# Optimization experiments

Measured on AMD Instinct MI355X. Metric: run time of the kernel, lower is better.

Reference implementation:

```python
import jax, jax.numpy as jnp
import numpy as np

EMBED = 1024
HEADS = 16
HEAD_DIM = EMBED // HEADS


def setup_inputs() -> dict:
    key = jax.random.key(0)
    ks = jax.random.split(key, 9)
    B, S = 1, 4096
    scale = 1.0 / np.sqrt(EMBED)
    x = jax.random.normal(ks[0], (B, S, EMBED), dtype=jnp.float32)
    # nn.Linear weights stored as [out, in]; we store transposed [in, out] for x @ W
    Wq = jax.random.uniform(ks[1], (EMBED, EMBED), jnp.float32, -scale, scale)
    bq = jax.random.uniform(ks[2], (EMBED,), jnp.float32, -scale, scale)
    Wk = jax.random.uniform(ks[3], (EMBED, EMBED), jnp.float32, -scale, scale)
    bk = jax.random.uniform(ks[4], (EMBED,), jnp.float32, -scale, scale)
    Wv = jax.random.uniform(ks[5], (EMBED, EMBED), jnp.float32, -scale, scale)
    bv = jax.random.uniform(ks[6], (EMBED,), jnp.float32, -scale, scale)
    Wo = jax.random.uniform(ks[7], (EMBED, EMBED), jnp.float32, -scale, scale)
    bo = jax.random.uniform(ks[8], (EMBED,), jnp.float32, -scale, scale)
    return {"x": x, "Wq": Wq, "bq": bq, "Wk": Wk, "bk": bk,
            "Wv": Wv, "bv": bv, "Wo": Wo, "bo": bo}


def reference(x, Wq, bq, Wk, bk, Wv, bv, Wo, bo):
    B, S, E = x.shape
    H, D = HEADS, HEAD_DIM
    # projections
    Q = (x @ Wq + bq).reshape(B, S, H, D).transpose(0, 2, 1, 3)  # [B,H,S,D]
    K = (x @ Wk + bk).reshape(B, S, H, D).transpose(0, 2, 1, 3)
    V = (x @ Wv + bv).reshape(B, S, H, D).transpose(0, 2, 1, 3)
    # unfused attention: full [B,H,S,S] score matrix, matching the torch module
    scores = jnp.einsum('bhqd,bhkd->bhqk', Q, K) / jnp.sqrt(jnp.float32(D)).astype(x.dtype)
    probs = jax.nn.softmax(scores, axis=-1)
    out = jnp.einsum('bhqk,bhkd->bhqd', probs, V)  # [B,H,S,D]
    out = out.transpose(0, 2, 1, 3).reshape(B, S, E)
    return out @ Wo + bo
```

## Files before the change

kernel.cpp:

```cpp
#include <hip/hip_runtime.h>


constexpr int Sq = 4096;
constexpr int Ee = 1024;
constexpr int Hh = 16;
constexpr int Dh = 64;

typedef _Float16 half8 __attribute__((ext_vector_type(8)));
typedef _Float16 half4 __attribute__((ext_vector_type(4)));
typedef _Float16 half2t __attribute__((ext_vector_type(2)));
typedef float f32x4 __attribute__((ext_vector_type(4)));

__device__ __forceinline__ unsigned short f2h(float f) {
  _Float16 h = (_Float16)f;
  return *reinterpret_cast<unsigned short*>(&h);
}

__device__ __forceinline__ half2t pk(float a, float b) {
  return __builtin_bit_cast(half2t, __builtin_amdgcn_cvt_pkrtz(a, b));
}

__device__ __forceinline__ void gload16(const void* g, void* l) {
  __builtin_amdgcn_global_load_lds(
      (const __attribute__((address_space(1))) void*)g,
      (__attribute__((address_space(3))) void*)l, 16, 0, 0);
}

__global__ void k_prep(const float* __restrict__ x,
                       const float* __restrict__ Wq, const float* __restrict__ Wk,
                       const float* __restrict__ Wv, const float* __restrict__ Wo,
                       unsigned short* __restrict__ xb,
                       unsigned short* __restrict__ Wqt, unsigned short* __restrict__ Wkt,
                       unsigned short* __restrict__ Wvt, unsigned short* __restrict__ Wot) {
  int b = blockIdx.x, t = threadIdx.x;
  if (b < 4096) {
    int i = b * 256 + t;
    float4 v = reinterpret_cast<const float4*>(x)[i];
    ushort4 o;
    o.x = f2h(v.x); o.y = f2h(v.y); o.z = f2h(v.z); o.w = f2h(v.w);
    reinterpret_cast<ushort4*>(xb)[i] = o;
    return;
  }
  __shared__ unsigned short tile[64][65];
  int r = b - 4096;
  int wi = r >> 8, ti = r & 255;
  const float* W = (wi == 0) ? Wq : (wi == 1) ? Wk : (wi == 2) ? Wv : Wo;
  unsigned short* Wt = (wi == 0) ? Wqt : (wi == 1) ? Wkt : (wi == 2) ? Wvt : Wot;
  int kb = (ti & 15) * 64, nb = (ti >> 4) * 64;
  int r0 = t >> 4, c4 = (t & 15) * 4;
  for (int i = 0; i < 4; i++) {
    int row = r0 + i * 16;
    float4 v = *reinterpret_cast<const float4*>(W + (size_t)(kb + row) * Ee + nb + c4);
    tile[row][c4 + 0] = f2h(v.x); tile[row][c4 + 1] = f2h(v.y);
    tile[row][c4 + 2] = f2h(v.z); tile[row][c4 + 3] = f2h(v.w);
  }
  __syncthreads();
  for (int i = 0; i < 4; i++) {
    int nrow = r0 + i * 16;
    ushort4 o;
    o.x = tile[c4 + 0][nrow]; o.y = tile[c4 + 1][nrow];
    o.z = tile[c4 + 2][nrow]; o.w = tile[c4 + 3][nrow];
    *reinterpret_cast<ushort4*>(Wt + (size_t)(nb + nrow) * Ee + kb + c4) = o;
  }
}

__global__ __launch_bounds__(256) void k_gemm(
    const unsigned short* __restrict__ A,
    const unsigned short* __restrict__ W0, const unsigned short* __restrict__ W1,
    const unsigned short* __restrict__ W2,
    const float* __restrict__ b0, const float* __restrict__ b1, const float* __restrict__ b2,
    void* d0, void* d1, void* d2, int mode) {
  __shared__ __align__(16) unsigned short Al[128 * 64];
  __shared__ __align__(16) unsigned short Bl[128 * 64];
  const unsigned short* Wt; const float* bias; void* dst;
  if (blockIdx.z == 0)      { Wt = W0; bias = b0; dst = d0; }
  else if (blockIdx.z == 1) { Wt = W1; bias = b1; dst = d1; }
  else                      { Wt = W2; bias = b2; dst = d2; }

  int t = threadIdx.x;
  int w = t >> 6, L = t & 63, quad = L >> 4, c = L & 15;
  int m0 = blockIdx.x * 128, n0 = blockIdx.y * 128;
  int wm = w >> 1, wn = w & 1;

  f32x4 zero = {0.f, 0.f, 0.f, 0.f};
  f32x4 acc[4][4];
#pragma unroll
  for (int i = 0; i < 4; i++)
#pragma unroll
    for (int j = 0; j < 4; j++) acc[i][j] = zero;

  for (int k0 = 0; k0 < 1024; k0 += 64) {
    __syncthreads();
#pragma unroll
    for (int i = 0; i < 4; i++) {
      int ch = i * 256 + t;
      int row = ch >> 3, kgs = ch & 7, kg = kgs ^ (row & 7);
      gload16(A + (size_t)(m0 + row) * 1024 + k0 + kg * 8, &Al[ch * 8]);
    }
#pragma unroll
    for (int i = 0; i < 4; i++) {
      int ch = i * 256 + t;
      int row = ch >> 3, kgs = ch & 7, kg = kgs ^ (row & 7);
      gload16(Wt + (size_t)(n0 + row) * 1024 + k0 + kg * 8, &Bl[ch * 8]);
    }
    __syncthreads();
#pragma unroll
    for (int ks = 0; ks < 2; ks++) {
      half8 af[4], bfr[4];
#pragma unroll
      for (int i = 0; i < 4; i++) {
        int row = wm * 64 + i * 16 + c;
        int kg = (quad + 4 * ks) ^ (row & 7);
        af[i] = *reinterpret_cast<const half8*>(&Al[row * 64 + kg * 8]);
      }
#pragma unroll
      for (int j = 0; j < 4; j++) {
        int row = wn * 64 + j * 16 + c;
        int kg = (quad + 4 * ks) ^ (row & 7);
        bfr[j] = *reinterpret_cast<const half8*>(&Bl[row * 64 + kg * 8]);
      }
#pragma unroll
      for (int i = 0; i < 4; i++)
#pragma unroll
        for (int j = 0; j < 4; j++)
          acc[i][j] = __builtin_amdgcn_mfma_f32_16x16x32_f16(af[i], bfr[j], acc[i][j], 0, 0, 0);
    }
  }

  if (mode == 0 && blockIdx.z == 2) {
    unsigned short* Vt = (unsigned short*)dst;
#pragma unroll
    for (int j = 0; j < 4; j++) {
      int n = n0 + wn * 64 + j * 16 + c;
      int hh = n >> 6, d = n & 63;
      float bv = bias[n];
#pragma unroll
      for (int i = 0; i < 4; i++) {
        int pos = m0 + wm * 64 + (i >> 1) * 32 + quad * 8 + (i & 1) * 4;
        half4 hv;
#pragma unroll
        for (int r = 0; r < 4; r++) hv[r] = (_Float16)(acc[i][j][r] + bv);
        *reinterpret_cast<half4*>(&Vt[(size_t)hh * Dh * Sq + (size_t)d * Sq + pos]) = hv;
      }
    }
    return;
  }

  float sc = (mode == 0 && blockIdx.z == 0) ? 0.18033688011112042f : 1.0f;
#pragma unroll
  for (int j = 0; j < 4; j++) {
    int n = n0 + wn * 64 + j * 16 + c;
    float bv = bias[n];
#pragma unroll
    for (int i = 0; i < 4; i++) {
      int srow = m0 + wm * 64 + i * 16 + quad * 4;
#pragma unroll
      for (int r = 0; r < 4; r++) {
        float v = (acc[i][j][r] + bv) * sc;
        int s = srow + r;
        if (mode == 0) {
          ((unsigned short*)dst)[(size_t)(n >> 6) * Sq * Dh + (size_t)s * Dh + (n & 63)] = f2h(v);
        } else {
          ((float*)dst)[(size_t)s * 1024 + n] = v;
        }
      }
    }
  }
}

__global__ __launch_bounds__(512, 4) void k_attn(
    const unsigned short* __restrict__ Q, const unsigned short* __restrict__ K,
    const unsigned short* __restrict__ Vt, unsigned short* __restrict__ O) {
  __shared__ __align__(16) unsigned short SM[32768];
  int t = threadIdx.x;
  int w = t >> 6, L = t & 63, quad = L >> 4, c = L & 15;
  int wl = w & 3, par = w >> 2;
  int h = blockIdx.y, qb = blockIdx.x;
  const unsigned short* Qh = Q + (size_t)h * Sq * Dh;
  const unsigned short* Kh = K + (size_t)h * Sq * Dh;
  const unsigned short* Vth = Vt + (size_t)h * Dh * Sq;

  half8 qf[2][2];
#pragma unroll
  for (int qg = 0; qg < 2; qg++) {
    int qrow = qb * 128 + wl * 32 + qg * 16 + c;
#pragma unroll
    for (int ks = 0; ks < 2; ks++)
      qf[qg][ks] = *reinterpret_cast<const half8*>(Qh + (size_t)qrow * Dh + ks * 32 + quad * 8);
  }

  f32x4 zero = {0.f, 0.f, 0.f, 0.f};
  f32x4 o0[4], o1[4];
#pragma unroll
  for (int i = 0; i < 4; i++) { o0[i] = zero; o1[i] = zero; }
  f32x4 l0 = zero, l1 = zero;
  half8 ones8;
#pragma unroll
  for (int j = 0; j < 8; j++) ones8[j] = (_Float16)1.0f;

  int srow = t >> 3, skg = (t & 7) ^ (srow & 7);

#pragma unroll
  for (int p2 = 0; p2 < 2; p2++) {
    gload16(Kh + (size_t)(p2 * 64 + srow) * Dh + skg * 8, SM + (0 + p2) * 4096 + t * 8);
    gload16(Vth + (size_t)srow * Sq + p2 * 64 + skg * 8, SM + (2 + p2) * 4096 + t * 8);
  }

  for (int ob = 0; ob < 32; ob++) {
    __syncthreads();
    if (ob < 31) {
      int nb = ob + 1, buf = nb & 1;
#pragma unroll
      for (int p2 = 0; p2 < 2; p2++) {
        int tb = nb * 2 + p2;
        gload16(Kh + (size_t)(tb * 64 + srow) * Dh + skg * 8,
                SM + (buf * 4 + p2) * 4096 + t * 8);
        gload16(Vth + (size_t)srow * Sq + tb * 64 + skg * 8,
                SM + (buf * 4 + 2 + p2) * 4096 + t * 8);
      }
    }
    const unsigned short* Kc = SM + ((ob & 1) * 4 + par) * 4096;
    const unsigned short* Vc = SM + ((ob & 1) * 4 + 2 + par) * 4096;

    f32x4 st0[4], st1[4];
#pragma unroll
    for (int nt = 0; nt < 4; nt++) { st0[nt] = zero; st1[nt] = zero; }
#pragma unroll
    for (int ks = 0; ks < 2; ks++)
#pragma unroll
      for (int nt = 0; nt < 4; nt++) {
        int row = nt * 16 + c;
        half8 kfv = *reinterpret_cast<const half8*>(
            &Kc[row * 64 + (((ks * 4 + quad) ^ (row & 7))) * 8]);
        st0[nt] = __builtin_amdgcn_mfma_f32_16x16x32_f16(kfv, qf[0][ks], st0[nt], 0, 0, 0);
        st1[nt] = __builtin_amdgcn_mfma_f32_16x16x32_f16(kfv, qf[1][ks], st1[nt], 0, 0, 0);
      }

    half8 pB0[2], pB1[2];
#pragma unroll
    for (int n2 = 0; n2 < 2; n2++) {
      half2t a0 = pk(__builtin_amdgcn_exp2f(st0[2 * n2][0]), __builtin_amdgcn_exp2f(st0[2 * n2][1]));
      half2t a1 = pk(__builtin_amdgcn_exp2f(st0[2 * n2][2]), __builtin_amdgcn_exp2f(st0[2 * n2][3]));
      half2t a2 = pk(__builtin_amdgcn_exp2f(st0[2 * n2 + 1][0]), __builtin_amdgcn_exp2f(st0[2 * n2 + 1][1]));
      half2t a3 = pk(__builtin_amdgcn_exp2f(st0[2 * n2 + 1][2]), __builtin_amdgcn_exp2f(st0[2 * n2 + 1][3]));
      half4 alo = __builtin_shufflevector(a0, a1, 0, 1, 2, 3);
      half4 ahi = __builtin_shufflevector(a2, a3, 0, 1, 2, 3);
      pB0[n2] = __builtin_shufflevector(alo, ahi, 0, 1, 2, 3, 4, 5, 6, 7);
      half2t b0 = pk(__builtin_amdgcn_exp2f(st1[2 * n2][0]), __builtin_amdgcn_exp2f(st1[2 * n2][1]));
      half2t b1 = pk(__builtin_amdgcn_exp2f(st1[2 * n2][2]), __builtin_amdgcn_exp2f(st1[2 * n2][3]));
      half2t b2 = pk(__builtin_amdgcn_exp2f(st1[2 * n2 + 1][0]), __builtin_amdgcn_exp2f(st1[2 * n2 + 1][1]));
      half2t b3 = pk(__builtin_amdgcn_exp2f(st1[2 * n2 + 1][2]), __builtin_amdgcn_exp2f(st1[2 * n2 + 1][3]));
      half4 blo = __builtin_shufflevector(b0, b1, 0, 1, 2, 3);
      half4 bhi = __builtin_shufflevector(b2, b3, 0, 1, 2, 3);
      pB1[n2] = __builtin_shufflevector(blo, bhi, 0, 1, 2, 3, 4, 5, 6, 7);
      l0 = __builtin_amdgcn_mfma_f32_16x16x32_f16(ones8, pB0[n2], l0, 0, 0, 0);
      l1 = __builtin_amdgcn_mfma_f32_16x16x32_f16(ones8, pB1[n2], l1, 0, 0, 0);
    }

#pragma unroll
    for (int dt = 0; dt < 4; dt++) {
      int row = dt * 16 + c;
#pragma unroll
      for (int n2 = 0; n2 < 2; n2++) {
        half8 vv = *reinterpret_cast<const half8*>(
            &Vc[row * 64 + (((n2 * 4 + quad) ^ (row & 7))) * 8]);
        o0[dt] = __builtin_amdgcn_mfma_f32_16x16x32_f16(vv, pB0[n2], o0[dt], 0, 0, 0);
        o1[dt] = __builtin_amdgcn_mfma_f32_16x16x32_f16(vv, pB1[n2], o1[dt], 0, 0, 0);
      }
    }
  }

  __syncthreads();
  float* cb = (float*)SM;
  if (par == 1) {
#pragma unroll
    for (int v = 0; v < 4; v++) {
      *reinterpret_cast<f32x4*>(cb + ((wl * 9 + v) * 64 + L) * 4) = o0[v];
      *reinterpret_cast<f32x4*>(cb + ((wl * 9 + 4 + v) * 64 + L) * 4) = o1[v];
    }
    f32x4 lv = {l0[0], l1[0], 0.f, 0.f};
    *reinterpret_cast<f32x4*>(cb + ((wl * 9 + 8) * 64 + L) * 4) = lv;
  }
  __syncthreads();
  if (par == 0) {
#pragma unroll
    for (int v = 0; v < 4; v++) {
      o0[v] += *reinterpret_cast<const f32x4*>(cb + ((wl * 9 + v) * 64 + L) * 4);
      o1[v] += *reinterpret_cast<const f32x4*>(cb + ((wl * 9 + 4 + v) * 64 + L) * 4);
    }
    f32x4 lv = *reinterpret_cast<const f32x4*>(cb + ((wl * 9 + 8) * 64 + L) * 4);
    float lt0 = l0[0] + lv[0], lt1 = l1[0] + lv[1];

#pragma unroll
    for (int qg = 0; qg < 2; qg++) {
      float inv = 1.f / (qg ? lt1 : lt0);
      f32x4* oo = qg ? o1 : o0;
      int q = qb * 128 + wl * 32 + qg * 16 + c;
#pragma unroll
      for (int dt = 0; dt < 4; dt++) {
        half4 hv;
#pragma unroll
        for (int r = 0; r < 4; r++) hv[r] = (_Float16)(oo[dt][r] * inv);
        *reinterpret_cast<half4*>(&O[(size_t)q * 1024 + h * 64 + dt * 16 + quad * 4]) = hv;
      }
    }
  }
}

extern "C" void kernel_launch(void* const* d_in, const int* in_sizes, int n_in,
                              void* d_out, int out_size, void* d_ws, size_t ws_size,
                              hipStream_t stream) {
  const float* x  = (const float*)d_in[0];
  const float* Wq = (const float*)d_in[1];
  const float* bq = (const float*)d_in[2];
  const float* Wk = (const float*)d_in[3];
  const float* bk = (const float*)d_in[4];
  const float* Wv = (const float*)d_in[5];
  const float* bv = (const float*)d_in[6];
  const float* Wo = (const float*)d_in[7];
  const float* bo = (const float*)d_in[8];

  char* ws = (char*)d_ws;
  const size_t MB = 1u << 20;
  unsigned short* xb  = (unsigned short*)(ws);
  unsigned short* Wqt = (unsigned short*)(ws + 8 * MB);
  unsigned short* Wkt = (unsigned short*)(ws + 10 * MB);
  unsigned short* Wvt = (unsigned short*)(ws + 12 * MB);
  unsigned short* Wot = (unsigned short*)(ws + 14 * MB);
  unsigned short* Qb  = (unsigned short*)(ws + 16 * MB);
  unsigned short* Kb  = (unsigned short*)(ws + 24 * MB);
  unsigned short* Vtg = (unsigned short*)(ws + 32 * MB);
  unsigned short* Ob  = (unsigned short*)(ws + 40 * MB);

  k_prep<<<5120, 256, 0, stream>>>(x, Wq, Wk, Wv, Wo, xb, Wqt, Wkt, Wvt, Wot);
  k_gemm<<<dim3(32, 8, 3), 256, 0, stream>>>(xb, Wqt, Wkt, Wvt, bq, bk, bv,
                                             (void*)Qb, (void*)Kb, (void*)Vtg, 0);
  k_attn<<<dim3(32, 16), 512, 0, stream>>>(Qb, Kb, Vtg, Ob);
  k_gemm<<<dim3(32, 8, 1), 256, 0, stream>>>(Ob, Wot, Wot, Wot, bo, bo, bo,
                                             d_out, d_out, d_out, 1);
}
```

Measured before the change: 236.5 us.

## Swap MFMA operands for vectorized GEMM epilogue stores; precompute attention LDS offsets

The GEMM k-loop moves into a templated helper that can swap MFMA operand order, so the accumulator layout puts four consecutive output columns in each lane. This lets the Q/K and output-projection epilogues write half4/float4 vectors and load bias as vectors instead of doing scalar strided stores. In the attention kernel, the per-iteration LDS swizzle offsets are computed once before the loop, and the main loop is unrolled by two with constant buffer offsets, which removes per-iteration address math and the buffer-parity computation. The cost is more code size and a few extra registers for the offset arrays.

```diff
diff --git a/kernel.cpp b/kernel.cpp
--- a/kernel.cpp
+++ b/kernel.cpp
@@ -10,6 +10,8 @@
 typedef _Float16 half4 __attribute__((ext_vector_type(4)));
 typedef _Float16 half2t __attribute__((ext_vector_type(2)));
 typedef float f32x4 __attribute__((ext_vector_type(4)));
+
+union U8 { half8 v8; half2t h2[4]; };
 
 __device__ __forceinline__ unsigned short f2h(float f) {
   _Float16 h = (_Float16)f;
@@ -64,6 +66,54 @@
   }
 }
 
+template <bool TR>
+__device__ __forceinline__ void gemm_kloop(
+    const unsigned short* __restrict__ A, const unsigned short* __restrict__ Wt,
+    unsigned short* Al, unsigned short* Bl,
+    int m0, int n0, int t, int wm, int wn, int quad, int c, f32x4 (&acc)[4][4]) {
+  for (int k0 = 0; k0 < 1024; k0 += 64) {
+    __syncthreads();
+#pragma unroll
+    for (int i = 0; i < 4; i++) {
+      int ch = i * 256 + t;
+      int row = ch >> 3, kg = (ch & 7) ^ (row & 7);
+      gload16(A + (size_t)(m0 + row) * 1024 + k0 + kg * 8, &Al[ch * 8]);
+    }
+#pragma unroll
+    for (int i = 0; i < 4; i++) {
+      int ch = i * 256 + t;
+      int row = ch >> 3, kg = (ch & 7) ^ (row & 7);
+      gload16(Wt + (size_t)(n0 + row) * 1024 + k0 + kg * 8, &Bl[ch * 8]);
+    }
+    __syncthreads();
+#pragma unroll
+    for (int ks = 0; ks < 2; ks++) {
+      half8 af[4], bfr[4];
+#pragma unroll
+      for (int i = 0; i < 4; i++) {
+        int row = wm * 64 + i * 16 + c;
+        int kg = (quad + 4 * ks) ^ (row & 7);
+        af[i] = *reinterpret_cast<const half8*>(&Al[row * 64 + kg * 8]);
+      }
+#pragma unroll
+      for (int j = 0; j < 4; j++) {
+        int row = wn * 64 + j * 16 + c;
+        int kg = (quad + 4 * ks) ^ (row & 7);
+        bfr[j] = *reinterpret_cast<const half8*>(&Bl[row * 64 + kg * 8]);
+      }
+#pragma unroll
+      for (int i = 0; i < 4; i++)
+#pragma unroll
+        for (int j = 0; j < 4; j++) {
+          if (TR)
+            acc[j][i] = __builtin_amdgcn_mfma_f32_16x16x32_f16(bfr[j], af[i], acc[j][i], 0, 0, 0);
+          else
+            acc[i][j] = __builtin_amdgcn_mfma_f32_16x16x32_f16(af[i], bfr[j], acc[i][j], 0, 0, 0);
+        }
+    }
+  }
+}
+
 __global__ __launch_bounds__(256) void k_gemm(
     const unsigned short* __restrict__ A,
     const unsigned short* __restrict__ W0, const unsigned short* __restrict__ W1,
@@ -89,81 +139,57 @@
 #pragma unroll
     for (int j = 0; j < 4; j++) acc[i][j] = zero;
 
-  for (int k0 = 0; k0 < 1024; k0 += 64) {
-    __syncthreads();
-#pragma unroll
-    for (int i = 0; i < 4; i++) {
-      int ch = i * 256 + t;
-      int row = ch >> 3, kgs = ch & 7, kg = kgs ^ (row & 7);
-      gload16(A + (size_t)(m0 + row) * 1024 + k0 + kg * 8, &Al[ch * 8]);
-    }
-#pragma unroll
-    for (int i = 0; i < 4; i++) {
-      int ch = i * 256 + t;
-      int row = ch >> 3, kgs = ch & 7, kg = kgs ^ (row & 7);
-      gload16(Wt + (size_t)(n0 + row) * 1024 + k0 + kg * 8, &Bl[ch * 8]);
-    }
-    __syncthreads();
-#pragma unroll
-    for (int ks = 0; ks < 2; ks++) {
-      half8 af[4], bfr[4];
+  bool tr = (mode == 1) || (blockIdx.z < 2);
+  if (tr) gemm_kloop<true>(A, Wt, Al, Bl, m0, n0, t, wm, wn, quad, c, acc);
+  else    gemm_kloop<false>(A, Wt, Al, Bl, m0, n0, t, wm, wn, quad, c, acc);
+
+  if (mode == 1) {
+    float* out = (float*)dst;
+#pragma unroll
+    for (int j = 0; j < 4; j++) {
+      int nb4 = n0 + wn * 64 + j * 16 + quad * 4;
+      f32x4 b4 = *reinterpret_cast<const f32x4*>(bias + nb4);
 #pragma unroll
       for (int i = 0; i < 4; i++) {
-        int row = wm * 64 + i * 16 + c;
-        int kg = (quad + 4 * ks) ^ (row & 7);
-        af[i] = *reinterpret_cast<const half8*>(&Al[row * 64 + kg * 8]);
-      }
-#pragma unroll
-      for (int j = 0; j < 4; j++) {
-        int row = wn * 64 + j * 16 + c;
-        int kg = (quad + 4 * ks) ^ (row & 7);
-        bfr[j] = *reinterpret_cast<const half8*>(&Bl[row * 64 + kg * 8]);
-      }
-#pragma unroll
-      for (int i = 0; i < 4; i++)
-#pragma unroll
-        for (int j = 0; j < 4; j++)
-          acc[i][j] = __builtin_amdgcn_mfma_f32_16x16x32_f16(af[i], bfr[j], acc[i][j], 0, 0, 0);
-    }
-  }
-
-  if (mode == 0 && blockIdx.z == 2) {
-    unsigned short* Vt = (unsigned short*)dst;
+        int s = m0 + wm * 64 + i * 16 + c;
+        f32x4 v = acc[j][i] + b4;
+        *reinterpret_cast<f32x4*>(out + (size_t)s * 1024 + nb4) = v;
+      }
+    }
+    return;
+  }
+  if (blockIdx.z < 2) {
+    float sc = (blockIdx.z == 0) ? 0.18033688011112042f : 1.0f;
+    unsigned short* qk = (unsigned short*)dst;
 #pragma unroll
     for (int j = 0; j < 4; j++) {
-      int n = n0 + wn * 64 + j * 16 + c;
-      int hh = n >> 6, d = n & 63;
-      float bv = bias[n];
+      int nb4 = n0 + wn * 64 + j * 16 + quad * 4;
+      int hh = nb4 >> 6, d = nb4 & 63;
+      f32x4 b4 = *reinterpret_cast<const f32x4*>(bias + nb4);
 #pragma unroll
       for (int i = 0; i < 4; i++) {
-        int pos = m0 + wm * 64 + (i >> 1) * 32 + quad * 8 + (i & 1) * 4;
+        int s = m0 + wm * 64 + i * 16 + c;
         half4 hv;
 #pragma unroll
-        for (int r = 0; r < 4; r++) hv[r] = (_Float16)(acc[i][j][r] + bv);
-        *reinterpret_cast<half4*>(&Vt[(size_t)hh * Dh * Sq + (size_t)d * Sq + pos]) = hv;
+        for (int r = 0; r < 4; r++) hv[r] = (_Float16)((acc[j][i][r] + b4[r]) * sc);
+        *reinterpret_cast<half4*>(&qk[(size_t)hh * Sq * Dh + (size_t)s * Dh + d]) = hv;
       }
     }
     return;
   }
-
-  float sc = (mode == 0 && blockIdx.z == 0) ? 0.18033688011112042f : 1.0f;
+  unsigned short* Vt = (unsigned short*)dst;
 #pragma unroll
   for (int j = 0; j < 4; j++) {
     int n = n0 + wn * 64 + j * 16 + c;
+    int hh = n >> 6, d = n & 63;
     float bv = bias[n];
 #pragma unroll
     for (int i = 0; i < 4; i++) {
-      int srow = m0 + wm * 64 + i * 16 + quad * 4;
-#pragma unroll
-      for (int r = 0; r < 4; r++) {
-        float v = (acc[i][j][r] + bv) * sc;
-        int s = srow + r;
-        if (mode == 0) {
-          ((unsigned short*)dst)[(size_t)(n >> 6) * Sq * Dh + (size_t)s * Dh + (n & 63)] = f2h(v);
-        } else {
-          ((float*)dst)[(size_t)s * 1024 + n] = v;
-        }
-      }
+      int pos = m0 + wm * 64 + (i >> 1) * 32 + quad * 8 + (i & 1) * 4;
+      half4 hv;
+#pragma unroll
+      for (int r = 0; r < 4; r++) hv[r] = (_Float16)(acc[i][j][r] + bv);
+      *reinterpret_cast<half4*>(&Vt[(size_t)hh * Dh * Sq + (size_t)d * Sq + pos]) = hv;
     }
   }
 }
@@ -198,30 +224,33 @@
 #pragma unroll
   for (int j = 0; j < 8; j++) ones8[j] = (_Float16)1.0f;
 
+  int koff[2][4], voff[4][2];
+#pragma unroll
+  for (int ks = 0; ks < 2; ks++)
+#pragma unroll
+    for (int nt = 0; nt < 4; nt++) {
+      int row = nt * 16 + c;
+      koff[ks][nt] = par * 4096 + row * 64 + (((ks * 4 + quad) ^ (row & 7)) * 8);
+    }
+#pragma unroll
+  for (int dt = 0; dt < 4; dt++)
+#pragma unroll
+    for (int n2 = 0; n2 < 2; n2++) {
+      int row = dt * 16 + c;
+      voff[dt][n2] = (2 + par) * 4096 + row * 64 + (((n2 * 4 + quad) ^ (row & 7)) * 8);
+    }
+
   int srow = t >> 3, skg = (t & 7) ^ (srow & 7);
+  const unsigned short* Kg = Kh + srow * Dh + skg * 8;
+  const unsigned short* Vg = Vth + (size_t)srow * Sq + skg * 8;
 
 #pragma unroll
   for (int p2 = 0; p2 < 2; p2++) {
-    gload16(Kh + (size_t)(p2 * 64 + srow) * Dh + skg * 8, SM + (0 + p2) * 4096 + t * 8);
-    gload16(Vth + (size_t)srow * Sq + p2 * 64 + skg * 8, SM + (2 + p2) * 4096 + t * 8);
-  }
-
-  for (int ob = 0; ob < 32; ob++) {
-    __syncthreads();
-    if (ob < 31) {
-      int nb = ob + 1, buf = nb & 1;
-#pragma unroll
-      for (int p2 = 0; p2 < 2; p2++) {
-        int tb = nb * 2 + p2;
-        gload16(Kh + (size_t)(tb * 64 + srow) * Dh + skg * 8,
-                SM + (buf * 4 + p2) * 4096 + t * 8);
-        gload16(Vth + (size_t)srow * Sq + tb * 64 + skg * 8,
-                SM + (buf * 4 + 2 + p2) * 4096 + t * 8);
-      }
-    }
-    const unsigned short* Kc = SM + ((ob & 1) * 4 + par) * 4096;
-    const unsigned short* Vc = SM + ((ob & 1) * 4 + 2 + par) * 4096;
-
+    gload16(Kg + p2 * 4096, &SM[p2 * 4096 + t * 8]);
+    gload16(Vg + p2 * 64, &SM[(2 + p2) * 4096 + t * 8]);
+  }
+
+  auto body = [&](int BUFOFF) {
     f32x4 st0[4], st1[4];
 #pragma unroll
     for (int nt = 0; nt < 4; nt++) { st0[nt] = zero; st1[nt] = zero; }
@@ -229,45 +258,59 @@
     for (int ks = 0; ks < 2; ks++)
 #pragma unroll
       for (int nt = 0; nt < 4; nt++) {
-        int row = nt * 16 + c;
-        half8 kfv = *reinterpret_cast<const half8*>(
-            &Kc[row * 64 + (((ks * 4 + quad) ^ (row & 7))) * 8]);
+        half8 kfv = *reinterpret_cast<const half8*>(&SM[koff[ks][nt] + BUFOFF]);
         st0[nt] = __builtin_amdgcn_mfma_f32_16x16x32_f16(kfv, qf[0][ks], st0[nt], 0, 0, 0);
         st1[nt] = __builtin_amdgcn_mfma_f32_16x16x32_f16(kfv, qf[1][ks], st1[nt], 0, 0, 0);
       }
-
     half8 pB0[2], pB1[2];
 #pragma unroll
     for (int n2 = 0; n2 < 2; n2++) {
-      half2t a0 = pk(__builtin_amdgcn_exp2f(st0[2 * n2][0]), __builtin_amdgcn_exp2f(st0[2 * n2][1]));
-      half2t a1 = pk(__builtin_amdgcn_exp2f(st0[2 * n2][2]), __builtin_amdgcn_exp2f(st0[2 * n2][3]));
-      half2t a2 = pk(__builtin_amdgcn_exp2f(st0[2 * n2 + 1][0]), __builtin_amdgcn_exp2f(st0[2 * n2 + 1][1]));
-      half2t a3 = pk(__builtin_amdgcn_exp2f(st0[2 * n2 + 1][2]), __builtin_amdgcn_exp2f(st0[2 * n2 + 1][3]));
-      half4 alo = __builtin_shufflevector(a0, a1, 0, 1, 2, 3);
-      half4 ahi = __builtin_shufflevector(a2, a3, 0, 1, 2, 3);
-      pB0[n2] = __builtin_shufflevector(alo, ahi, 0, 1, 2, 3, 4, 5, 6, 7);
-      half2t b0 = pk(__builtin_amdgcn_exp2f(st1[2 * n2][0]), __builtin_amdgcn_exp2f(st1[2 * n2][1]));
-      half2t b1 = pk(__builtin_amdgcn_exp2f(st1[2 * n2][2]), __builtin_amdgcn_exp2f(st1[2 * n2][3]));
-      half2t b2 = pk(__builtin_amdgcn_exp2f(st1[2 * n2 + 1][0]), __builtin_amdgcn_exp2f(st1[2 * n2 + 1][1]));
-      half2t b3 = pk(__builtin_amdgcn_exp2f(st1[2 * n2 + 1][2]), __builtin_amdgcn_exp2f(st1[2 * n2 + 1][3]));
-      half4 blo = __builtin_shufflevector(b0, b1, 0, 1, 2, 3);
-      half4 bhi = __builtin_shufflevector(b2, b3, 0, 1, 2, 3);
-      pB1[n2] = __builtin_shufflevector(blo, bhi, 0, 1, 2, 3, 4, 5, 6, 7);
+      U8 u;
+      u.h2[0] = pk(__builtin_amdgcn_exp2f(st0[2 * n2][0]), __builtin_amdgcn_exp2f(st0[2 * n2][1]));
+      u.h2[1] = pk(__builtin_amdgcn_exp2f(st0[2 * n2][2]), __builtin_amdgcn_exp2f(st0[2 * n2][3]));
+      u.h2[2] = pk(__builtin_amdgcn_exp2f(st0[2 * n2 + 1][0]), __builtin_amdgcn_exp2f(st0[2 * n2 + 1][1]));
+      u.h2[3] = pk(__builtin_amdgcn_exp2f(st0[2 * n2 + 1][2]), __builtin_amdgcn_exp2f(st0[2 * n2 + 1][3]));
+      pB0[n2] = u.v8;
+      U8 v;
+      v.h2[0] = pk(__builtin_amdgcn_exp2f(st1[2 * n2][0]), __builtin_amdgcn_exp2f(st1[2 * n2][1]));
+      v.h2[1] = pk(__builtin_amdgcn_exp2f(st1[2 * n2][2]), __builtin_amdgcn_exp2f(st1[2 * n2][3]));
+      v.h2[2] = pk(__builtin_amdgcn_exp2f(st1[2 * n2 + 1][0]), __builtin_amdgcn_exp2f(st1[2 * n2 + 1][1]));
+      v.h2[3] = pk(__builtin_amdgcn_exp2f(st1[2 * n2 + 1][2]), __builtin_amdgcn_exp2f(st1[2 * n2 + 1][3]));
+      pB1[n2] = v.v8;
       l0 = __builtin_amdgcn_mfma_f32_16x16x32_f16(ones8, pB0[n2], l0, 0, 0, 0);
       l1 = __builtin_amdgcn_mfma_f32_16x16x32_f16(ones8, pB1[n2], l1, 0, 0, 0);
     }
-
-#pragma unroll
-    for (int dt = 0; dt < 4; dt++) {
-      int row = dt * 16 + c;
+#pragma unroll
+    for (int dt = 0; dt < 4; dt++)
 #pragma unroll
       for (int n2 = 0; n2 < 2; n2++) {
-        half8 vv = *reinterpret_cast<const half8*>(
-            &Vc[row * 64 + (((n2 * 4 + quad) ^ (row & 7))) * 8]);
+        half8 vv = *reinterpret_cast<const half8*>(&SM[voff[dt][n2] + BUFOFF]);
         o0[dt] = __builtin_amdgcn_mfma_f32_16x16x32_f16(vv, pB0[n2], o0[dt], 0, 0, 0);
         o1[dt] = __builtin_amdgcn_mfma_f32_16x16x32_f16(vv, pB1[n2], o1[dt], 0, 0, 0);
       }
-    }
+  };
+
+  for (int ob2 = 0; ob2 < 16; ob2++) {
+    __syncthreads();
+    {
+      int tb = 4 * ob2 + 2;
+#pragma unroll
+      for (int p2 = 0; p2 < 2; p2++) {
+        gload16(Kg + (size_t)(tb + p2) * 4096, &SM[16384 + p2 * 4096 + t * 8]);
+        gload16(Vg + (tb + p2) * 64, &SM[16384 + (2 + p2) * 4096 + t * 8]);
+      }
+    }
+    body(0);
+    __syncthreads();
+    if (ob2 < 15) {
+      int tb = 4 * ob2 + 4;
+#pragma unroll
+      for (int p2 = 0; p2 < 2; p2++) {
+        gload16(Kg + (size_t)(tb + p2) * 4096, &SM[p2 * 4096 + t * 8]);
+        gload16(Vg + (tb + p2) * 64, &SM[(2 + p2) * 4096 + t * 8]);
+      }
+    }
+    body(16384);
   }
 
   __syncthreads();
```

New measurement: 233.8 us. About the same (-1.2%).
